# Performance work log

Measured on AMD Instinct MI355X. Metric: run time of the kernel, lower is better.

## Reference

```python
import jax, jax.numpy as jnp
import numpy as np

D_MODEL, N_HEADS, D_FF = 1024, 16, 2752
B, S = 2, 2048
EPS = 1e-5


def setup_inputs() -> dict:
    key = jax.random.key(0)
    ks = jax.random.split(key, 8)
    def w(k, fan_in, fan_out):
        std = np.sqrt(2.0 / (fan_in + fan_out))
        return jax.random.truncated_normal(k, -3.0, 3.0, (fan_in, fan_out), jnp.float32) * std
    return {
        "x": jax.random.normal(ks[0], (B, S, D_MODEL), jnp.float32),
        "g1": jnp.ones((D_MODEL,), jnp.float32),
        "g2": jnp.ones((D_MODEL,), jnp.float32),
        "w_q": w(ks[1], D_MODEL, D_MODEL),
        "w_k": w(ks[2], D_MODEL, D_MODEL),
        "w_v": w(ks[3], D_MODEL, D_MODEL),
        "w_o": w(ks[4], D_MODEL, D_MODEL),
        "w1": w(ks[5], D_MODEL, D_FF),
        "w2": w(ks[6], D_FF, D_MODEL),
        "w3": w(ks[7], D_MODEL, D_FF),
    }


def rmsnorm(x, g):
    xf = x.astype(jnp.float32)
    rms = jnp.sqrt(jnp.mean(xf * xf, axis=-1, keepdims=True) + EPS)
    return (xf / rms).astype(x.dtype) * g


def reference(x, g1, g2, w_q, w_k, w_v, w_o, w1, w2, w3):
    b, s, d = x.shape
    h = N_HEADS
    dh = d // h

    # --- causal multi-head self-attention on norm1(x) ---
    xn = rmsnorm(x, g1)
    q = (xn @ w_q).reshape(b, s, h, dh).transpose(0, 2, 1, 3)  # b h s d
    k = (xn @ w_k).reshape(b, s, h, dh).transpose(0, 2, 1, 3)
    v = (xn @ w_v).reshape(b, s, h, dh).transpose(0, 2, 1, 3)

    scores = jnp.einsum('bhqd,bhkd->bhqk', q, k) / jnp.sqrt(jnp.float32(dh))
    causal = jnp.tril(jnp.ones((s, s), dtype=bool))
    scores = jnp.where(causal, scores, -jnp.inf)
    probs = jax.nn.softmax(scores, axis=-1)
    attn = jnp.einsum('bhqk,bhkd->bhqd', probs, v)
    attn = attn.transpose(0, 2, 1, 3).reshape(b, s, d)
    h_res = x + attn @ w_o

    # --- SwiGLU FFN on norm2(h) ---
    hn = rmsnorm(h_res, g2)
    x1 = hn @ w1
    gate = x1 * jax.nn.sigmoid(x1)
    ffn = (gate * (hn @ w3)) @ w2
    return h_res + ffn
```

## Files before the change

### kernel.cpp

```cpp
#include <hip/hip_runtime.h>
#include <hip/hip_bf16.h>

typedef unsigned short u16;
typedef __bf16 bf16x8 __attribute__((ext_vector_type(8)));
typedef float  f32x4  __attribute__((ext_vector_type(4)));

#define D_MODEL 1024
#define SEQ     2048
#define NHEAD   16
#define DHEAD   64
#define QKVS    3072

__device__ __forceinline__ float bflo(unsigned u) { return __uint_as_float(u << 16); }
__device__ __forceinline__ float bfhi(unsigned u) { return __uint_as_float(u & 0xffff0000u); }
__device__ __forceinline__ u16 f2bf(float f) {
    unsigned u = __float_as_uint(f);
    u += 0x7fffu + ((u >> 16) & 1u);
    return (u16)(u >> 16);
}
__device__ __forceinline__ u16 f2bf_fast(float f) {
    return (u16)((__float_as_uint(f) + 0x8000u) >> 16);
}
__device__ __forceinline__ void gld_lds16(const u16* g, u16* l) {
    __builtin_amdgcn_global_load_lds((const __attribute__((address_space(1))) void*)g,
                                     (__attribute__((address_space(3))) void*)l, 16, 0, 0);
}

__global__ void detect_k(const unsigned* __restrict__ g1w, int* __restrict__ flag) {
    int c = 0;
#pragma unroll
    for (int i = 0; i < 8; ++i) c += (g1w[i] == 0x3F800000u) ? 1 : 0;
    *flag = (c >= 4) ? 1 : 0;
}

__global__ __launch_bounds__(256) void tp_k(const void* __restrict__ in_, u16* __restrict__ out,
                                            int K, int N, const int* __restrict__ flagp) {
    __shared__ u16 tile[32][33];
    const int f32 = *flagp;
    int k0 = blockIdx.x * 32, n0 = blockIdx.y * 32;
    int tx = threadIdx.x & 31, ty = threadIdx.x >> 5;
#pragma unroll
    for (int i = 0; i < 32; i += 8) {
        int nn = n0 + tx;
        u16 v = 0;
        if (nn < N) {
            size_t idx = (size_t)(k0 + ty + i) * N + nn;
            v = f32 ? f2bf(((const float*)in_)[idx]) : ((const u16*)in_)[idx];
        }
        tile[ty + i][tx] = v;
    }
    __syncthreads();
#pragma unroll
    for (int i = 0; i < 32; i += 8)
        out[(size_t)(n0 + ty + i) * K + (k0 + tx)] = tile[tx][ty + i];
}

__global__ __launch_bounds__(256) void tpm_k(const void* __restrict__ a, const void* __restrict__ b,
                                             const void* __restrict__ c, u16* __restrict__ out,
                                             int K, int N, int outStride,
                                             const int* __restrict__ flagp) {
    __shared__ u16 tile[32][33];
    const void* in_ = (blockIdx.z == 0) ? a : (blockIdx.z == 1) ? b : c;
    u16* o = out + (size_t)blockIdx.z * outStride;
    const int f32 = *flagp;
    int k0 = blockIdx.x * 32, n0 = blockIdx.y * 32;
    int tx = threadIdx.x & 31, ty = threadIdx.x >> 5;
#pragma unroll
    for (int i = 0; i < 32; i += 8) {
        int nn = n0 + tx;
        u16 v = 0;
        if (nn < N) {
            size_t idx = (size_t)(k0 + ty + i) * N + nn;
            v = f32 ? f2bf(((const float*)in_)[idx]) : ((const u16*)in_)[idx];
        }
        tile[ty + i][tx] = v;
    }
    __syncthreads();
#pragma unroll
    for (int i = 0; i < 32; i += 8)
        o[(size_t)(n0 + ty + i) * K + (k0 + tx)] = tile[tx][ty + i];
}

__global__ __launch_bounds__(256) void rms_k(const void* __restrict__ x_, const void* __restrict__ g_,
                                             u16* __restrict__ o, const int* __restrict__ flagp,
                                             int x_raw) {
    const size_t row = blockIdx.x;
    const int f32 = *flagp;
    const int xf32 = f32 & x_raw;
    int t = threadIdx.x;
    float f0, f1, f2, f3, g0, g1, g2, g3;
    if (xf32) {
        float4 xv = *(const float4*)((const float*)x_ + row * D_MODEL + t * 4);
        f0 = xv.x; f1 = xv.y; f2 = xv.z; f3 = xv.w;
    } else {
        uint2 u = *(const uint2*)((const u16*)x_ + row * D_MODEL + t * 4);
        f0 = bflo(u.x); f1 = bfhi(u.x); f2 = bflo(u.y); f3 = bfhi(u.y);
    }
    if (f32) {
        float4 gv = *(const float4*)((const float*)g_ + t * 4);
        g0 = gv.x; g1 = gv.y; g2 = gv.z; g3 = gv.w;
    } else {
        uint2 gu = *(const uint2*)((const u16*)g_ + t * 4);
        g0 = bflo(gu.x); g1 = bfhi(gu.x); g2 = bflo(gu.y); g3 = bfhi(gu.y);
    }
    float s = f0 * f0 + f1 * f1 + f2 * f2 + f3 * f3;
#pragma unroll
    for (int off = 32; off > 0; off >>= 1) s += __shfl_xor(s, off, 64);
    __shared__ float ps[4];
    if ((t & 63) == 0) ps[t >> 6] = s;
    __syncthreads();
    float tot = ps[0] + ps[1] + ps[2] + ps[3];
    float rinv = rsqrtf(tot * (1.0f / D_MODEL) + 1e-5f);
    float fv[4] = {f0, f1, f2, f3};
    float gv2[4] = {g0, g1, g2, g3};
    u16 r[4];
#pragma unroll
    for (int i = 0; i < 4; ++i)
        r[i] = f2bf(fv[i] * rinv * gv2[i]);
    uint2 w;
    w.x = (unsigned)r[0] | ((unsigned)r[1] << 16);
    w.y = (unsigned)r[2] | ((unsigned)r[3] << 16);
    *(uint2*)(o + row * D_MODEL + t * 4) = w;
}

__global__ __launch_bounds__(256) void gemm_k(const u16* __restrict__ A, int lda,
                                              const u16* __restrict__ Bt, int ldb,
                                              u16* C, int ldc,
                                              const void* res, int K, int mode,
                                              const int* __restrict__ flagp, int res_raw,
                                              int out32) {
    __shared__ alignas(16) u16 As[128 * 32];
    __shared__ alignas(16) u16 Bs[128 * 32];
    const int t = threadIdx.x;
    const int rf32 = (mode == 1 && res_raw) ? *flagp : 0;
    const int wid = t >> 6, lane = t & 63;
    const int wm = (wid >> 1) * 64, wn = (wid & 1) * 64;
    const int m0 = blockIdx.x * 128, n0 = blockIdx.y * 128;
    const int fr = lane & 15, quad = lane >> 4;

    f32x4 acc[4][4] = {};

    for (int k0 = 0; k0 < K; k0 += 32) {
        __syncthreads();
#pragma unroll
        for (int r = 0; r < 2; ++r) {
            int e = r * 256 + t;
            int row = e >> 2, c = (e & 3) * 8;
            gld_lds16(A  + (size_t)(m0 + row) * lda + k0 + c, As + e * 8);
            gld_lds16(Bt + (size_t)(n0 + row) * ldb + k0 + c, Bs + e * 8);
        }
        __syncthreads();
        bf16x8 af[4], bfr[4];
#pragma unroll
        for (int i = 0; i < 4; ++i) {
            af[i]  = *(const bf16x8*)(As + (wm + i * 16 + fr) * 32 + quad * 8);
            bfr[i] = *(const bf16x8*)(Bs + (wn + i * 16 + fr) * 32 + quad * 8);
        }
#pragma unroll
        for (int i = 0; i < 4; ++i)
#pragma unroll
            for (int j = 0; j < 4; ++j)
                acc[i][j] = __builtin_amdgcn_mfma_f32_16x16x32_bf16(af[i], bfr[j], acc[i][j], 0, 0, 0);
    }

#pragma unroll
    for (int i = 0; i < 4; ++i)
#pragma unroll
        for (int j = 0; j < 4; ++j)
#pragma unroll
            for (int r2 = 0; r2 < 4; ++r2) {
                int row = m0 + wm + i * 16 + quad * 4 + r2;
                int col = n0 + wn + j * 16 + fr;
                size_t idx = (size_t)row * ldc + col;
                float v = acc[i][j][r2];
                if (mode == 1) {
                    float rv = rf32 ? ((const float*)res)[idx]
                                    : __uint_as_float((unsigned)((const u16*)res)[idx] << 16);
                    v += rv;
                }
                if (out32) ((float*)C)[idx] = v;
                else       C[idx] = f2bf(v);
            }
}

__global__ __launch_bounds__(256) void gemm64_k(const u16* __restrict__ A, int lda,
                                                const u16* __restrict__ Bt, int ldb,
                                                u16* C, int ldc,
                                                const void* res, int K, int mode,
                                                const int* __restrict__ flagp, int res_raw,
                                                int out32) {
    __shared__ alignas(16) u16 As[64 * 32];
    __shared__ alignas(16) u16 Bs[128 * 32];
    const int t = threadIdx.x;
    const int rf32 = (mode == 1 && res_raw) ? *flagp : 0;
    const int wid = t >> 6, lane = t & 63;
    const int wm = (wid >> 1) * 32, wn = (wid & 1) * 64;
    const int m0 = blockIdx.x * 64, n0 = blockIdx.y * 128;
    const int fr = lane & 15, quad = lane >> 4;

    f32x4 acc[2][4] = {};

    for (int k0 = 0; k0 < K; k0 += 32) {
        __syncthreads();
        {
            int row = t >> 2, c = (t & 3) * 8;
            gld_lds16(A + (size_t)(m0 + row) * lda + k0 + c, As + t * 8);
        }
#pragma unroll
        for (int r = 0; r < 2; ++r) {
            int e = r * 256 + t;
            int row = e >> 2, c = (e & 3) * 8;
            gld_lds16(Bt + (size_t)(n0 + row) * ldb + k0 + c, Bs + e * 8);
        }
        __syncthreads();
        bf16x8 af[2], bfr[4];
#pragma unroll
        for (int i = 0; i < 2; ++i)
            af[i] = *(const bf16x8*)(As + (wm + i * 16 + fr) * 32 + quad * 8);
#pragma unroll
        for (int j = 0; j < 4; ++j)
            bfr[j] = *(const bf16x8*)(Bs + (wn + j * 16 + fr) * 32 + quad * 8);
#pragma unroll
        for (int i = 0; i < 2; ++i)
#pragma unroll
            for (int j = 0; j < 4; ++j)
                acc[i][j] = __builtin_amdgcn_mfma_f32_16x16x32_bf16(af[i], bfr[j], acc[i][j], 0, 0, 0);
    }

#pragma unroll
    for (int i = 0; i < 2; ++i)
#pragma unroll
        for (int j = 0; j < 4; ++j)
#pragma unroll
            for (int r2 = 0; r2 < 4; ++r2) {
                int row = m0 + wm + i * 16 + quad * 4 + r2;
                int col = n0 + wn + j * 16 + fr;
                size_t idx = (size_t)row * ldc + col;
                float v = acc[i][j][r2];
                if (mode == 1) {
                    float rv = rf32 ? ((const float*)res)[idx]
                                    : __uint_as_float((unsigned)((const u16*)res)[idx] << 16);
                    v += rv;
                }
                if (out32) ((float*)C)[idx] = v;
                else       C[idx] = f2bf(v);
            }
}

__global__ __launch_bounds__(256, 2) void ffn_k(const u16* __restrict__ A,
                                                const u16* __restrict__ B1t,
                                                const u16* __restrict__ B3t,
                                                u16* __restrict__ G, int ldg) {
    __shared__ alignas(16) u16 As[128 * 32];
    __shared__ alignas(16) u16 B1s[128 * 32];
    __shared__ alignas(16) u16 B3s[128 * 32];
    const int t = threadIdx.x;
    const int wid = t >> 6, lane = t & 63;
    const int wm = (wid >> 1) * 64, wn = (wid & 1) * 64;
    const int m0 = blockIdx.x * 128, n0 = blockIdx.y * 128;
    const int fr = lane & 15, quad = lane >> 4;

    f32x4 acc1[4][4] = {};
    f32x4 acc3[4][4] = {};

    for (int k0 = 0; k0 < 1024; k0 += 32) {
        __syncthreads();
#pragma unroll
        for (int r = 0; r < 2; ++r) {
            int e = r * 256 + t;
            int row = e >> 2, c = (e & 3) * 8;
            gld_lds16(A   + (size_t)(m0 + row) * 1024 + k0 + c, As  + e * 8);
            gld_lds16(B1t + (size_t)(n0 + row) * 1024 + k0 + c, B1s + e * 8);
            gld_lds16(B3t + (size_t)(n0 + row) * 1024 + k0 + c, B3s + e * 8);
        }
        __syncthreads();
        bf16x8 af[4], b1[4], b3[4];
#pragma unroll
        for (int i = 0; i < 4; ++i) {
            af[i] = *(const bf16x8*)(As  + (wm + i * 16 + fr) * 32 + quad * 8);
            b1[i] = *(const bf16x8*)(B1s + (wn + i * 16 + fr) * 32 + quad * 8);
            b3[i] = *(const bf16x8*)(B3s + (wn + i * 16 + fr) * 32 + quad * 8);
        }
#pragma unroll
        for (int i = 0; i < 4; ++i)
#pragma unroll
            for (int j = 0; j < 4; ++j) {
                acc1[i][j] = __builtin_amdgcn_mfma_f32_16x16x32_bf16(af[i], b1[j], acc1[i][j], 0, 0, 0);
                acc3[i][j] = __builtin_amdgcn_mfma_f32_16x16x32_bf16(af[i], b3[j], acc3[i][j], 0, 0, 0);
            }
    }

#pragma unroll
    for (int i = 0; i < 4; ++i)
#pragma unroll
        for (int j = 0; j < 4; ++j)
#pragma unroll
            for (int r2 = 0; r2 < 4; ++r2) {
                int row = m0 + wm + i * 16 + quad * 4 + r2;
                int col = n0 + wn + j * 16 + fr;
                float xv = acc1[i][j][r2];
                xv = fminf(fmaxf(xv, -60.f), 60.f);
                float sg = xv / (1.0f + __expf(-xv));
                G[(size_t)row * ldg + col] = f2bf(sg * acc3[i][j][r2]);
            }
}

__global__ __launch_bounds__(256) void vtp_k(const u16* __restrict__ qkv, u16* __restrict__ vt) {
    __shared__ u16 tile[32][33];
    const int bh = blockIdx.z, b = bh >> 4, h = bh & 15;
    const int s0 = blockIdx.x * 32, d0 = blockIdx.y * 32;
    const int tx = threadIdx.x & 31, ty = threadIdx.x >> 5;
#pragma unroll
    for (int i = 0; i < 32; i += 8)
        tile[ty + i][tx] = qkv[(size_t)(b * SEQ + s0 + ty + i) * QKVS + 2048 + h * 64 + d0 + tx];
    __syncthreads();
#pragma unroll
    for (int i = 0; i < 32; i += 8)
        vt[(size_t)(bh * 64 + d0 + ty + i) * SEQ + s0 + tx] = tile[tx][ty + i];
}

#define KPAD 68
#define PPAD 72
__constant__ int JC[38]  = {5,4, 15,15,15,15, 11,11,11, 7,7, 14,14, 10, 3, 14,14,
                            13,13,13,13, 12,12, 10,10, 9,9, 6,6, 12,12, 9, 8,8,8, 2, 1, 0};
__constant__ int JK0[38] = {0,0, 0,8,16,24, 0,8,16, 0,8, 7,22, 14, 0, 0,15,
                            0,7,14,21, 6,19, 0,7, 6,13, 0,7, 0,13, 0, 0,6,12, 0, 0, 0};
__constant__ int JKN[38] = {12,10, 8,8,8,8, 8,8,8, 8,8, 8,8, 8, 8, 7,7,
                            7,7,7,7, 7,7, 7,7, 7,7, 7,7, 6,6, 6, 6,6,6, 6, 4, 2};
__constant__ int JSL[38] = {-1,-1, 28,29,30,31, 13,14,15, 2,3, 25,27, 12, -1, 24,26,
                            20,21,22,23, 17,19, 10,11, 8,9, 0,1, 16,18, 7, 4,5,6, -1, -1, -1};

__global__ __launch_bounds__(256) void fattn_k(const u16* __restrict__ QKV, const u16* __restrict__ Vt,
                                               u16* __restrict__ O,
                                               u16* __restrict__ pOa, u16* __restrict__ pOb,
                                               float* __restrict__ pL) {
    __shared__ alignas(16) u16 Ks[64 * KPAD];
    __shared__ alignas(16) u16 Vs[64 * KPAD];
    __shared__ alignas(16) u16 Ps[4 * 32 * PPAD];

    const int bh = blockIdx.y;
    const int j = blockIdx.x;
    const int chunk = JC[j], kt0 = JK0[j], ktn = JKN[j], sl = JSL[j];
    const int partial = (sl >= 0);
    const int slot = bh * 32 + sl;

    const size_t baseqk = ((size_t)(bh >> 4) * SEQ) * QKVS + (size_t)(bh & 15) * DHEAD;
    const size_t baseo  = ((size_t)(bh >> 4) * SEQ) * D_MODEL + (size_t)(bh & 15) * DHEAD;
    const size_t vtbase = (size_t)bh * 64 * SEQ;
    const u16* Qp = QKV + baseqk;
    const u16* Kp = QKV + baseqk + 1024;
    const int r0 = chunk * 128;
    const int t = threadIdx.x, w = t >> 6, lane = t & 63;
    const int fr = lane & 15, quad = lane >> 4;

    bf16x8 qa[2][2];
#pragma unroll
    for (int s = 0; s < 2; ++s) {
        const u16* qp = Qp + (size_t)(r0 + w * 32 + s * 16 + fr) * QKVS + quad * 8;
        qa[s][0] = *(const bf16x8*)(qp);
        qa[s][1] = *(const bf16x8*)(qp + 32);
    }

    f32x4 oacc[2][4] = {};
    float lp[2][4] = {};
    u16* Pw = Ps + w * 32 * PPAD;
    const float sc = 0.125f * 1.44269504f;
    const int qrow_min = r0 + w * 32;

    for (int kt = kt0; kt < kt0 + ktn; ++kt) {
        const int kb = kt * 64;
        __syncthreads();
#pragma unroll
        for (int it = 0; it < 2; ++it) {
            int e = it * 256 + t;
            int rr = e >> 3, cc = (e & 7) * 8;
            *(uint4*)(Ks + rr * KPAD + cc) = *(const uint4*)(Kp + (size_t)(kb + rr) * QKVS + cc);
            *(uint4*)(Vs + rr * KPAD + cc) = *(const uint4*)(Vt + vtbase + (size_t)rr * SEQ + kb + cc);
        }
        __syncthreads();

#pragma unroll
        for (int s = 0; s < 2; ++s) {
            f32x4 sac[4] = {};
#pragma unroll
            for (int n = 0; n < 4; ++n) {
                bf16x8 kf0 = *(const bf16x8*)(Ks + (n * 16 + fr) * KPAD + quad * 8);
                bf16x8 kf1 = *(const bf16x8*)(Ks + (n * 16 + fr) * KPAD + 32 + quad * 8);
                sac[n] = __builtin_amdgcn_mfma_f32_16x16x32_bf16(qa[s][0], kf0, sac[n], 0, 0, 0);
                sac[n] = __builtin_amdgcn_mfma_f32_16x16x32_bf16(qa[s][1], kf1, sac[n], 0, 0, 0);
            }
            const int smin = qrow_min + s * 16;
            if (kb + 64 <= smin) {
#pragma unroll
                for (int n = 0; n < 4; ++n)
#pragma unroll
                    for (int r = 0; r < 4; ++r) {
                        float p = exp2f(fminf(sac[n][r] * sc, 126.f));
                        lp[s][r] += p;
                        Pw[(s * 16 + quad * 4 + r) * PPAD + n * 16 + fr] = f2bf_fast(p);
                    }
            } else {
                const int qb_s = smin + quad * 4;
#pragma unroll
                for (int n = 0; n < 4; ++n) {
                    int key = kb + n * 16 + fr;
#pragma unroll
                    for (int r = 0; r < 4; ++r) {
                        float p = (key <= qb_s + r) ? exp2f(fminf(sac[n][r] * sc, 126.f)) : 0.f;
                        lp[s][r] += p;
                        Pw[(s * 16 + quad * 4 + r) * PPAD + n * 16 + fr] = f2bf_fast(p);
                    }
                }
            }
        }
        __threadfence_block();
        bf16x8 vf0[4], vf1[4];
#pragma unroll
        for (int n = 0; n < 4; ++n) {
            vf0[n] = *(const bf16x8*)(Vs + (n * 16 + fr) * KPAD + quad * 8);
            vf1[n] = *(const bf16x8*)(Vs + (n * 16 + fr) * KPAD + 32 + quad * 8);
        }
#pragma unroll
        for (int s = 0; s < 2; ++s) {
            bf16x8 pa0 = *(const bf16x8*)(Pw + (s * 16 + fr) * PPAD + quad * 8);
            bf16x8 pa1 = *(const bf16x8*)(Pw + (s * 16 + fr) * PPAD + 32 + quad * 8);
#pragma unroll
            for (int n = 0; n < 4; ++n) {
                oacc[s][n] = __builtin_amdgcn_mfma_f32_16x16x32_bf16(pa0, vf0[n], oacc[s][n], 0, 0, 0);
                oacc[s][n] = __builtin_amdgcn_mfma_f32_16x16x32_bf16(pa1, vf1[n], oacc[s][n], 0, 0, 0);
            }
        }
    }

#pragma unroll
    for (int s = 0; s < 2; ++s)
#pragma unroll
        for (int r = 0; r < 4; ++r) {
            float v = lp[s][r];
            v += __shfl_xor(v, 1, 64);
            v += __shfl_xor(v, 2, 64);
            v += __shfl_xor(v, 4, 64);
            v += __shfl_xor(v, 8, 64);
            lp[s][r] = v;
        }
    if (!partial) {
#pragma unroll
        for (int s = 0; s < 2; ++s)
#pragma unroll
            for (int r = 0; r < 4; ++r) {
                float linv = 1.0f / lp[s][r];
                u16* op = O + baseo + (size_t)(qrow_min + s * 16 + quad * 4 + r) * D_MODEL;
#pragma unroll
                for (int n = 0; n < 4; ++n)
                    op[n * 16 + fr] = f2bf(oacc[s][n][r] * linv);
            }
    } else {
        u16* po = (slot < 512) ? (pOa + (size_t)slot * 8192)
                               : (pOb + (size_t)(slot - 512) * 8192);
#pragma unroll
        for (int s = 0; s < 2; ++s)
#pragma unroll
            for (int r = 0; r < 4; ++r) {
                int rl = w * 32 + s * 16 + quad * 4 + r;
#pragma unroll
                for (int n = 0; n < 4; ++n)
                    po[rl * 64 + n * 16 + fr] = f2bf(oacc[s][n][r]);
                if (fr == 0) pL[slot * 128 + rl] = lp[s][r];
            }
    }
}

__global__ __launch_bounds__(256) void fcomb_k(const u16* __restrict__ pOa, const u16* __restrict__ pOb,
                                               const float* __restrict__ pL,
                                               u16* __restrict__ O) {
    const int id = blockIdx.x;
    const int bh = id / 10, pc = id % 10;
    const int chunk = 6 + pc;
    const int np = 2 + (pc >= 2) + (pc >= 6);
    const int pref = 2 * (pc < 2 ? pc : 2) + 3 * (pc < 2 ? 0 : (pc < 6 ? pc - 2 : 4))
                   + 4 * (pc < 6 ? 0 : pc - 6);
    const int base = bh * 32 + pref;
    const size_t baseo = ((size_t)(bh >> 4) * SEQ) * D_MODEL + (size_t)(bh & 15) * DHEAD;
    const int r0 = chunk * 128;
    for (int e = threadIdx.x; e < 8192; e += 256) {
        int row = e >> 6, d = e & 63;
        float o = 0.f, l = 0.f;
        for (int p = 0; p < np; ++p) {
            int S = base + p;
            const u16* ptr = (S < 512) ? (pOa + (size_t)S * 8192)
                                       : (pOb + (size_t)(S - 512) * 8192);
            o += __uint_as_float((unsigned)ptr[e] << 16);
            l += pL[S * 128 + row];
        }
        O[baseo + (size_t)(r0 + row) * D_MODEL + d] = f2bf(o / l);
    }
}

extern "C" void kernel_launch(void* const* d_in, const int* in_sizes, int n_in,
                              void* d_out, int out_size, void* d_ws, size_t ws_size,
                              hipStream_t stream) {
    const void* x  = d_in[0];
    const void* g1 = d_in[1];
    const void* g2 = d_in[2];
    const void* wq = d_in[3];
    const void* wk = d_in[4];
    const void* wv = d_in[5];
    const void* wo = d_in[6];
    const void* w1 = d_in[7];
    const void* w2 = d_in[8];
    const void* w3 = d_in[9];
    u16* ws  = (u16*)d_ws;

    u16*   xn    = ws;
    u16*   pOb   = ws;
    u16*   qkv   = ws + 4194304;
    u16*   gate  = ws + 4194304;
    u16*   pOa   = ws + 16777216;
    u16*   hres  = ws + 16777216;
    int*   flag  = (int*)(ws + 20971520);
    u16*   wqkvT = ws + 20971776;
    u16*   woT   = ws + 20971776;
    u16*   w2T   = ws + 20971776;
    float* pL    = (float*)(ws + 23789824);
    u16*   vt    = (u16*)d_out;
    u16*   attn  = (u16*)d_out + 4194304;
    u16*   w1T   = (u16*)d_out;
    u16*   w3T   = (u16*)d_out + 2883584;

    detect_k<<<1, 1, 0, stream>>>((const unsigned*)g1, flag);

    tpm_k<<<dim3(32, 32, 3), 256, 0, stream>>>(wq, wk, wv, wqkvT, 1024, 1024, 1048576, flag);
    rms_k<<<4096, 256, 0, stream>>>(x, g1, xn, flag, 1);

    gemm_k<<<dim3(32, 24), 256, 0, stream>>>(xn, 1024, wqkvT, 1024, qkv, QKVS, nullptr, 1024, 0, flag, 0, 0);

    tp_k<<<dim3(32, 32), 256, 0, stream>>>(wo, woT, 1024, 1024, flag);
    vtp_k<<<dim3(64, 2, 32), 256, 0, stream>>>(qkv, vt);
    fattn_k<<<dim3(38, 32), 256, 0, stream>>>(qkv, vt, attn, pOa, pOb, pL);
    fcomb_k<<<320, 256, 0, stream>>>(pOa, pOb, pL, attn);

    gemm64_k<<<dim3(64, 8), 256, 0, stream>>>(attn, 1024, woT, 1024, hres, 1024, x, 1024, 1, flag, 1, 0);

    rms_k<<<4096, 256, 0, stream>>>(hres, g2, xn, flag, 0);

    tpm_k<<<dim3(32, 88, 2), 256, 0, stream>>>(w1, w3, w3, w1T, 1024, 2752, 2883584, flag);
    tp_k<<<dim3(86, 32), 256, 0, stream>>>(w2, w2T, 2752, 1024, flag);

    ffn_k<<<dim3(32, 22), 256, 0, stream>>>(xn, w1T, w3T, gate, 2816);

    gemm64_k<<<dim3(64, 8), 256, 0, stream>>>(gate, 2816, w2T, 2752, (u16*)d_out, 1024, hres, 2752, 1, flag, 0, 1);
}
```

Baseline: 457.4 us.

## Double-buffer LDS tiles in GEMM and FFN kernels to overlap loads with MFMA

The three matmul kernels (gemm_k, gemm64_k, ffn_k) now keep two LDS buffers per operand. Each iteration issues the async global-to-LDS loads for the next K slice into the spare buffer, then runs the MFMAs on the current one, with one barrier per iteration instead of two. The aim is to hide global load latency behind matrix math. In exchange, LDS use per block doubles (48KB for ffn_k), which could limit how many blocks fit on each CU.

```diff
diff --git a/kernel.cpp b/kernel.cpp
--- a/kernel.cpp
+++ b/kernel.cpp
@@ -129,8 +129,8 @@
                                               const void* res, int K, int mode,
                                               const int* __restrict__ flagp, int res_raw,
                                               int out32) {
-    __shared__ alignas(16) u16 As[128 * 32];
-    __shared__ alignas(16) u16 Bs[128 * 32];
+    __shared__ alignas(16) u16 As[2][128 * 32];
+    __shared__ alignas(16) u16 Bs[2][128 * 32];
     const int t = threadIdx.x;
     const int rf32 = (mode == 1 && res_raw) ? *flagp : 0;
     const int wid = t >> 6, lane = t & 63;
@@ -140,27 +140,40 @@
 
     f32x4 acc[4][4] = {};
 
+#pragma unroll
+    for (int r = 0; r < 2; ++r) {
+        int e = r * 256 + t;
+        int row = e >> 2, c = (e & 3) * 8;
+        gld_lds16(A  + (size_t)(m0 + row) * lda + c, As[0] + e * 8);
+        gld_lds16(Bt + (size_t)(n0 + row) * ldb + c, Bs[0] + e * 8);
+    }
+    __syncthreads();
+    int cur = 0;
+
     for (int k0 = 0; k0 < K; k0 += 32) {
-        __syncthreads();
-#pragma unroll
-        for (int r = 0; r < 2; ++r) {
-            int e = r * 256 + t;
-            int row = e >> 2, c = (e & 3) * 8;
-            gld_lds16(A  + (size_t)(m0 + row) * lda + k0 + c, As + e * 8);
-            gld_lds16(Bt + (size_t)(n0 + row) * ldb + k0 + c, Bs + e * 8);
-        }
-        __syncthreads();
+        const int nk = k0 + 32;
+        if (nk < K) {
+#pragma unroll
+            for (int r = 0; r < 2; ++r) {
+                int e = r * 256 + t;
+                int row = e >> 2, c = (e & 3) * 8;
+                gld_lds16(A  + (size_t)(m0 + row) * lda + nk + c, As[cur ^ 1] + e * 8);
+                gld_lds16(Bt + (size_t)(n0 + row) * ldb + nk + c, Bs[cur ^ 1] + e * 8);
+            }
+        }
         bf16x8 af[4], bfr[4];
 #pragma unroll
         for (int i = 0; i < 4; ++i) {
-            af[i]  = *(const bf16x8*)(As + (wm + i * 16 + fr) * 32 + quad * 8);
-            bfr[i] = *(const bf16x8*)(Bs + (wn + i * 16 + fr) * 32 + quad * 8);
+            af[i]  = *(const bf16x8*)(As[cur] + (wm + i * 16 + fr) * 32 + quad * 8);
+            bfr[i] = *(const bf16x8*)(Bs[cur] + (wn + i * 16 + fr) * 32 + quad * 8);
         }
 #pragma unroll
         for (int i = 0; i < 4; ++i)
 #pragma unroll
             for (int j = 0; j < 4; ++j)
                 acc[i][j] = __builtin_amdgcn_mfma_f32_16x16x32_bf16(af[i], bfr[j], acc[i][j], 0, 0, 0);
+        __syncthreads();
+        cur ^= 1;
     }
 
 #pragma unroll
@@ -189,8 +202,8 @@
                                                 const void* res, int K, int mode,
                                                 const int* __restrict__ flagp, int res_raw,
                                                 int out32) {
-    __shared__ alignas(16) u16 As[64 * 32];
-    __shared__ alignas(16) u16 Bs[128 * 32];
+    __shared__ alignas(16) u16 As[2][64 * 32];
+    __shared__ alignas(16) u16 Bs[2][128 * 32];
     const int t = threadIdx.x;
     const int rf32 = (mode == 1 && res_raw) ? *flagp : 0;
     const int wid = t >> 6, lane = t & 63;
@@ -200,31 +213,47 @@
 
     f32x4 acc[2][4] = {};
 
+    {
+        int row = t >> 2, c = (t & 3) * 8;
+        gld_lds16(A + (size_t)(m0 + row) * lda + c, As[0] + t * 8);
+    }
+#pragma unroll
+    for (int r = 0; r < 2; ++r) {
+        int e = r * 256 + t;
+        int row = e >> 2, c = (e & 3) * 8;
+        gld_lds16(Bt + (size_t)(n0 + row) * ldb + c, Bs[0] + e * 8);
+    }
+    __syncthreads();
+    int cur = 0;
+
     for (int k0 = 0; k0 < K; k0 += 32) {
-        __syncthreads();
-        {
-            int row = t >> 2, c = (t & 3) * 8;
-            gld_lds16(A + (size_t)(m0 + row) * lda + k0 + c, As + t * 8);
-        }
-#pragma unroll
-        for (int r = 0; r < 2; ++r) {
-            int e = r * 256 + t;
-            int row = e >> 2, c = (e & 3) * 8;
-            gld_lds16(Bt + (size_t)(n0 + row) * ldb + k0 + c, Bs + e * 8);
-        }
-        __syncthreads();
+        const int nk = k0 + 32;
+        if (nk < K) {
+            {
+                int row = t >> 2, c = (t & 3) * 8;
+                gld_lds16(A + (size_t)(m0 + row) * lda + nk + c, As[cur ^ 1] + t * 8);
+            }
+#pragma unroll
+            for (int r = 0; r < 2; ++r) {
+                int e = r * 256 + t;
+                int row = e >> 2, c = (e & 3) * 8;
+                gld_lds16(Bt + (size_t)(n0 + row) * ldb + nk + c, Bs[cur ^ 1] + e * 8);
+            }
+        }
         bf16x8 af[2], bfr[4];
 #pragma unroll
         for (int i = 0; i < 2; ++i)
-            af[i] = *(const bf16x8*)(As + (wm + i * 16 + fr) * 32 + quad * 8);
+            af[i] = *(const bf16x8*)(As[cur] + (wm + i * 16 + fr) * 32 + quad * 8);
 #pragma unroll
         for (int j = 0; j < 4; ++j)
-            bfr[j] = *(const bf16x8*)(Bs + (wn + j * 16 + fr) * 32 + quad * 8);
+            bfr[j] = *(const bf16x8*)(Bs[cur] + (wn + j * 16 + fr) * 32 + quad * 8);
 #pragma unroll
         for (int i = 0; i < 2; ++i)
 #pragma unroll
             for (int j = 0; j < 4; ++j)
                 acc[i][j] = __builtin_amdgcn_mfma_f32_16x16x32_bf16(af[i], bfr[j], acc[i][j], 0, 0, 0);
+        __syncthreads();
+        cur ^= 1;
     }
 
 #pragma unroll
@@ -251,9 +280,9 @@
                                                 const u16* __restrict__ B1t,
                                                 const u16* __restrict__ B3t,
                                                 u16* __restrict__ G, int ldg) {
-    __shared__ alignas(16) u16 As[128 * 32];
-    __shared__ alignas(16) u16 B1s[128 * 32];
-    __shared__ alignas(16) u16 B3s[128 * 32];
+    __shared__ alignas(16) u16 As[2][128 * 32];
+    __shared__ alignas(16) u16 B1s[2][128 * 32];
+    __shared__ alignas(16) u16 B3s[2][128 * 32];
     const int t = threadIdx.x;
     const int wid = t >> 6, lane = t & 63;
     const int wm = (wid >> 1) * 64, wn = (wid & 1) * 64;
@@ -263,23 +292,35 @@
     f32x4 acc1[4][4] = {};
     f32x4 acc3[4][4] = {};
 
+#pragma unroll
+    for (int r = 0; r < 2; ++r) {
+        int e = r * 256 + t;
+        int row = e >> 2, c = (e & 3) * 8;
+        gld_lds16(A   + (size_t)(m0 + row) * 1024 + c, As[0]  + e * 8);
+        gld_lds16(B1t + (size_t)(n0 + row) * 1024 + c, B1s[0] + e * 8);
+        gld_lds16(B3t + (size_t)(n0 + row) * 1024 + c, B3s[0] + e * 8);
+    }
+    __syncthreads();
+    int cur = 0;
+
     for (int k0 = 0; k0 < 1024; k0 += 32) {
-        __syncthreads();
-#pragma unroll
-        for (int r = 0; r < 2; ++r) {
-            int e = r * 256 + t;
-            int row = e >> 2, c = (e & 3) * 8;
-            gld_lds16(A   + (size_t)(m0 + row) * 1024 + k0 + c, As  + e * 8);
-            gld_lds16(B1t + (size_t)(n0 + row) * 1024 + k0 + c, B1s + e * 8);
-            gld_lds16(B3t + (size_t)(n0 + row) * 1024 + k0 + c, B3s + e * 8);
-        }
-        __syncthreads();
+        const int nk = k0 + 32;
+        if (nk < 1024) {
+#pragma unroll
+            for (int r = 0; r < 2; ++r) {
+                int e = r * 256 + t;
+                int row = e >> 2, c = (e & 3) * 8;
+                gld_lds16(A   + (size_t)(m0 + row) * 1024 + nk + c, As[cur ^ 1]  + e * 8);
+                gld_lds16(B1t + (size_t)(n0 + row) * 1024 + nk + c, B1s[cur ^ 1] + e * 8);
+                gld_lds16(B3t + (size_t)(n0 + row) * 1024 + nk + c, B3s[cur ^ 1] + e * 8);
+            }
+        }
         bf16x8 af[4], b1[4], b3[4];
 #pragma unroll
         for (int i = 0; i < 4; ++i) {
-            af[i] = *(const bf16x8*)(As  + (wm + i * 16 + fr) * 32 + quad * 8);
-            b1[i] = *(const bf16x8*)(B1s + (wn + i * 16 + fr) * 32 + quad * 8);
-            b3[i] = *(const bf16x8*)(B3s + (wn + i * 16 + fr) * 32 + quad * 8);
+            af[i] = *(const bf16x8*)(As[cur]  + (wm + i * 16 + fr) * 32 + quad * 8);
+            b1[i] = *(const bf16x8*)(B1s[cur] + (wn + i * 16 + fr) * 32 + quad * 8);
+            b3[i] = *(const bf16x8*)(B3s[cur] + (wn + i * 16 + fr) * 32 + quad * 8);
         }
 #pragma unroll
         for (int i = 0; i < 4; ++i)
@@ -288,6 +329,8 @@
                 acc1[i][j] = __builtin_amdgcn_mfma_f32_16x16x32_bf16(af[i], b1[j], acc1[i][j], 0, 0, 0);
                 acc3[i][j] = __builtin_amdgcn_mfma_f32_16x16x32_bf16(af[i], b3[j], acc3[i][j], 0, 0, 0);
             }
+        __syncthreads();
+        cur ^= 1;
     }
 
 #pragma unroll
```

Measured after the change: 444.7 us. -2.8%, faster.
